# Kernel optimization log

Measured on AMD Instinct MI355X. Metric: run time of the kernel, lower is better.

Reference implementation:

```python
import jax, jax.numpy as jnp
import numpy as np
from jax import lax

V, E, H, K, T, B = 32000, 512, 512, 32, 256, 64
PAD_W = 0          # word_dict['PAD']
START, END, PAD_L = 30, 31, 0   # label_dict
NEG = -100000.0


def setup_inputs() -> dict:
    key = jax.random.key(0)
    ks = jax.random.split(key, 12)
    s = 1.0 / np.sqrt(H)
    tokens = jax.random.randint(ks[0], (T, B), 1, V, dtype=jnp.int32)   # >PAD_W -> mask all ones
    tags = jax.random.randint(ks[1], (T, B), 1, K - 2, dtype=jnp.int32)
    lengths = jnp.full((B,), T, dtype=jnp.int32)
    embed = jax.random.normal(ks[2], (V, E), jnp.float32) * 0.1
    wih0 = jax.random.uniform(ks[3], (2, 4 * H, E), jnp.float32, -s, s)
    whh0 = jax.random.uniform(ks[4], (2, 4 * H, H), jnp.float32, -s, s)
    b0 = jax.random.uniform(ks[5], (2, 4 * H), jnp.float32, -s, s)
    wih1 = jax.random.uniform(ks[6], (2, 4 * H, 2 * H), jnp.float32, -s, s)
    whh1 = jax.random.uniform(ks[7], (2, 4 * H, H), jnp.float32, -s, s)
    b1 = jax.random.uniform(ks[8], (2, 4 * H), jnp.float32, -s, s)
    lin_w = jax.random.uniform(ks[9], (K, 2 * H), jnp.float32, -s, s)
    lin_b = jax.random.uniform(ks[10], (K,), jnp.float32, -s, s)
    trans = jax.random.normal(ks[11], (K, K), jnp.float32)
    # replicate the torch transition init (same order of assignments)
    trans = trans.at[START, :].set(NEG)
    trans = trans.at[:, END].set(NEG)
    trans = trans.at[:, PAD_L].set(NEG)
    trans = trans.at[PAD_L, :].set(NEG)
    trans = trans.at[PAD_L, END].set(0.0)
    trans = trans.at[PAD_L, PAD_L].set(0.0)
    return dict(tokens=tokens, tags=tags, lengths=lengths, embed=embed,
                wih0=wih0, whh0=whh0, b0=b0, wih1=wih1, whh1=whh1, b1=b1,
                lin_w=lin_w, lin_b=lin_b, trans=trans)


def _lstm_dir(x, w_ih, w_hh, b, reverse):
    # x: [T,B,in] -> hs: [T,B,H]; gates precomputed as one big GEMM
    xp = jnp.einsum('tbi,gi->tbg', x, w_ih) + b  # [T,B,4H]
    h0 = jnp.zeros((x.shape[1], H), x.dtype)

    def step(carry, g_in):
        h, c = carry
        g = g_in + h @ w_hh.T
        i, f, gg, o = jnp.split(g, 4, axis=-1)  # torch gate order i,f,g,o
        c = jax.nn.sigmoid(f) * c + jax.nn.sigmoid(i) * jnp.tanh(gg)
        h = jax.nn.sigmoid(o) * jnp.tanh(c)
        return (h, c), h

    _, hs = lax.scan(step, (h0, h0), xp, reverse=reverse)
    return hs


def _bilstm_layer(x, wih, whh, b):
    return jnp.concatenate([_lstm_dir(x, wih[0], whh[0], b[0], False),
                            _lstm_dir(x, wih[1], whh[1], b[1], True)], axis=-1)


def reference(tokens, tags, lengths, embed, wih0, whh0, b0, wih1, whh1, b1,
              lin_w, lin_b, trans):
    mask = (tokens > PAD_W).astype(jnp.float32)  # [T,B]
    x = embed[tokens]                            # [T,B,E]
    x = _bilstm_layer(x, wih0, whh0, b0)
    x = _bilstm_layer(x, wih1, whh1, b1)
    feats = x @ lin_w.T + lin_b                  # [T,B,K]

    nB = tokens.shape[1]
    # ---- CRF forward algorithm: log Z(x) ----
    init = jnp.full((nB, K), NEG, feats.dtype).at[:, START].set(0.0)

    def step(score, inp):
        emit, m = inp  # [B,K], [B]
        # new[b,k] = logsumexp_j(score[b,j] + trans[k,j]) + emit[b,k]
        new = jax.nn.logsumexp(score[:, None, :] + trans[None, :, :], axis=2) + emit
        return jnp.where(m[:, None] > 0, new, score), None

    z, _ = lax.scan(step, init, (feats, mask))
    log_z = jax.nn.logsumexp(z + trans[END][None, :], axis=1)  # [B]

    # ---- gold path score (vectorized, masked deltas sum) ----
    start_row = jnp.full((1, nB), START, dtype=tags.dtype)
    te = jnp.concatenate([start_row, tags], axis=0)            # [T+1,B]
    trans_s = trans[te[1:], te[:-1]]                           # [T,B]
    emit_s = jnp.take_along_axis(feats, te[1:][..., None].astype(jnp.int32), axis=2)[..., 0]
    gold = jnp.sum(mask * (trans_s + emit_s), axis=0) + trans[END, te[-1]]

    return jnp.sum((log_z - gold) / lengths.astype(jnp.float32))
```

## Files before the change

kernel.cpp:

```cpp
#include <hip/hip_runtime.h>
#include <math.h>

#define T_STEPS 256
#define BATCH   64
#define HID     512
#define KTAGS   32
#define NEGV    -100000.0f
#define START_TAG 30
#define END_TAG   31

#define NBLK      256
#define SPIN_LIM  (1 << 26)
#define LAYER_DONE  300u
#define POISON_DONE 301u
#define POISON    0xFFFFFFFFFFFFFFFFULL

typedef __attribute__((ext_vector_type(8))) short short8;
typedef __attribute__((ext_vector_type(4))) float f32x4;

union V16 { uint4 u; short8 s; };
union HQ  { unsigned long long q[2]; short8 s; };

static __device__ __forceinline__ unsigned short f2b(float f) {
    unsigned u = __float_as_uint(f);
    return (unsigned short)((u + 0x7fffu + ((u >> 16) & 1u)) >> 16);
}
static __device__ __forceinline__ float b2f(unsigned short us) {
    return __uint_as_float(((unsigned)us) << 16);
}

__global__ __launch_bounds__(256) void init_zero(unsigned int* __restrict__ flags,
                                                 unsigned long long* __restrict__ hbuf,
                                                 float* __restrict__ out)
{
    int i = blockIdx.x * 256 + threadIdx.x;
    if (i < 131072)
        __hip_atomic_store(hbuf + i, POISON, __ATOMIC_RELAXED, __HIP_MEMORY_SCOPE_AGENT);
    if (i < 16384)
        __hip_atomic_store(flags + i, 0u, __ATOMIC_RELAXED, __HIP_MEMORY_SCOPE_AGENT);
    if (i == 0)
        __hip_atomic_store(out, 0.0f, __ATOMIC_RELAXED, __HIP_MEMORY_SCOPE_AGENT);
}

__global__ __launch_bounds__(256) void convert_embed(const float* __restrict__ src,
                                                     unsigned short* __restrict__ dst)
{
    long long i = ((long long)blockIdx.x * 256 + threadIdx.x) * 4;
    if (i >= (long long)32000 * 512) return;
    float4 v = *(const float4*)(src + i);
    ushort4 o;
    o.x = f2b(v.x); o.y = f2b(v.y); o.z = f2b(v.z); o.w = f2b(v.w);
    *(ushort4*)(dst + i) = o;
}

__global__ __launch_bounds__(256) void pack_w(const float* __restrict__ wih,
                                              const float* __restrict__ whh,
                                              int xK,
                                              unsigned short* __restrict__ wpack)
{
    const int xKt = xK >> 5, KT = xKt + 16;
    long long t = (long long)blockIdx.x * 256 + threadIdx.x;
    if (t >= (long long)2 * 64 * KT * 2 * 64) return;
    int lane = (int)(t & 63);
    long long rest = t >> 6;
    int nf = (int)(rest & 1); rest >>= 1;
    int kt = (int)(rest % KT); rest /= KT;
    int nt = (int)(rest % 64);
    int d  = (int)(rest / 64);
    int c = lane & 15, q = lane >> 4;
    int bc = nf * 16 + c;
    int r = (bc >> 3) * 512 + nt * 8 + (bc & 7);
    const float* src;
    if (kt < xKt) src = wih + ((long long)d * 2048 * xK + (long long)r * xK + kt * 32 + q * 8);
    else          src = whh + ((long long)d * 2048 * 512 + (long long)r * 512 + (kt - xKt) * 32 + q * 8);
    float4 v0 = *(const float4*)src;
    float4 v1 = *(const float4*)(src + 4);
    unsigned short o[8] = { f2b(v0.x), f2b(v0.y), f2b(v0.z), f2b(v0.w),
                            f2b(v1.x), f2b(v1.y), f2b(v1.z), f2b(v1.w) };
    *(uint4*)(wpack + t * 8) = *(const uint4*)o;
}

__global__ __launch_bounds__(256) void lstm_mfma(
    const int* __restrict__ tokens,
    const unsigned short* __restrict__ embB,
    const unsigned short* __restrict__ wp0,
    const unsigned short* __restrict__ wp1,
    const float* __restrict__ bb0, const float* __restrict__ bb1,
    unsigned short* __restrict__ hs0,
    unsigned short* __restrict__ hs1,
    unsigned long long* __restrict__ hbuf64,
    unsigned int* __restrict__ flags)
{
    __shared__ uint4 wldsH[2048];
    __shared__ float Gred[4][32][33];
    __shared__ float hsh[32][9];
    __shared__ int   tok_s[32];

    const int bid = blockIdx.x;
    const int d   = bid >> 7;
    const int bg  = (bid >> 6) & 1;
    const int nt  = bid & 63;
    const int tid = threadIdx.x;
    const int w    = tid >> 6;
    const int lane = tid & 63;
    const int lm = lane & 15, q = lane >> 4;
    const int brow = tid >> 3, hc = tid & 7;

    float creg = 0.0f;

    for (int l = 0; l < 2; ++l) {
        const int xK  = l ? 1024 : 512;
        const int xKt = xK >> 5;
        const int KT  = xKt + 16;
        const int nX  = xKt >> 2;
        const unsigned short* wp = (l ? wp1 : wp0) + (long long)(d * 64 + nt) * KT * 1024;
        const float* bia = (l ? bb1 : bb0) + (long long)d * 2048;
        unsigned short* hso = l ? hs1 : hs0;

        const uint4* wp4 = (const uint4*)wp;
        for (int j = tid; j < 2048; j += 256)
            wldsH[j] = wp4[xKt * 128 + j];

        float breg[4];
        #pragma unroll
        for (int g = 0; g < 4; ++g) breg[g] = bia[g * 512 + nt * 8 + hc];
        creg = 0.0f;
        __syncthreads();

        for (int s = 0; s < T_STEPS; ++s) {
            const int tt = d ? (T_STEPS - 1 - s) : s;

            if (l == 0 && tid < 32) tok_s[tid] = tokens[tt * BATCH + bg * 32 + tid];
            __syncthreads();

            HQ hq[4][2];
            const unsigned long long* hbq =
                hbuf64 + (long long)(((((s - 1) & 7) * 2 + d) * 2 + bg)) * 4096;
            if (s > 0) {
                #pragma unroll
                for (int i = 0; i < 4; ++i) {
                    const int kth = w * 4 + i;
                    #pragma unroll
                    for (int mt = 0; mt < 2; ++mt) {
                        const int base = (kth * 4 + q) * 64 + (mt * 16 + lm) * 2;
                        hq[i][mt].q[0] = __hip_atomic_load(hbq + base,     __ATOMIC_RELAXED, __HIP_MEMORY_SCOPE_AGENT);
                        hq[i][mt].q[1] = __hip_atomic_load(hbq + base + 1, __ATOMIC_RELAXED, __HIP_MEMORY_SCOPE_AGENT);
                    }
                }
            }

            f32x4 acc[2][2];
            #pragma unroll
            for (int mt = 0; mt < 2; ++mt)
                #pragma unroll
                for (int nf = 0; nf < 2; ++nf) acc[mt][nf] = (f32x4)0.0f;

            const unsigned short* xr[2];
            #pragma unroll
            for (int mt = 0; mt < 2; ++mt) {
                int m = mt * 16 + lm;
                if (l == 0) xr[mt] = embB + (long long)tok_s[m] * 512;
                else        xr[mt] = hs0 + ((long long)tt * 64 + bg * 32 + m) * 1024;
            }

            for (int i = 0; i < nX; ++i) {
                const int kt = w * nX + i;
                V16 av[2], bv[2];
                #pragma unroll
                for (int mt = 0; mt < 2; ++mt)
                    av[mt].u = *(const uint4*)(xr[mt] + kt * 32 + q * 8);
                #pragma unroll
                for (int nf = 0; nf < 2; ++nf)
                    bv[nf].u = *(const uint4*)(wp + ((long long)kt * 128 + nf * 64 + lane) * 8);
                #pragma unroll
                for (int mt = 0; mt < 2; ++mt)
                    #pragma unroll
                    for (int nf = 0; nf < 2; ++nf)
                        acc[mt][nf] = __builtin_amdgcn_mfma_f32_16x16x32_bf16(av[mt].s, bv[nf].s, acc[mt][nf], 0, 0, 0);
            }

            if (s > 0) {
                int n = 0;
                for (;;) {
                    int bad = 0;
                    #pragma unroll
                    for (int i = 0; i < 4; ++i) {
                        const int kth = w * 4 + i;
                        #pragma unroll
                        for (int mt = 0; mt < 2; ++mt) {
                            const int base = (kth * 4 + q) * 64 + (mt * 16 + lm) * 2;
                            if (hq[i][mt].q[0] == POISON) {
                                hq[i][mt].q[0] = __hip_atomic_load(hbq + base,     __ATOMIC_RELAXED, __HIP_MEMORY_SCOPE_AGENT);
                                bad = 1;
                            }
                            if (hq[i][mt].q[1] == POISON) {
                                hq[i][mt].q[1] = __hip_atomic_load(hbq + base + 1, __ATOMIC_RELAXED, __HIP_MEMORY_SCOPE_AGENT);
                                bad = 1;
                            }
                        }
                    }
                    if (!bad) break;
                    __builtin_amdgcn_s_sleep(1);
                    if (++n > SPIN_LIM) break;
                }

                #pragma unroll
                for (int i = 0; i < 4; ++i) {
                    const int kth = w * 4 + i;
                    V16 bv[2];
                    #pragma unroll
                    for (int nf = 0; nf < 2; ++nf)
                        bv[nf].u = wldsH[(kth * 2 + nf) * 64 + lane];
                    #pragma unroll
                    for (int mt = 0; mt < 2; ++mt)
                        #pragma unroll
                        for (int nf = 0; nf < 2; ++nf)
                            acc[mt][nf] = __builtin_amdgcn_mfma_f32_16x16x32_bf16(hq[i][mt].s, bv[nf].s, acc[mt][nf], 0, 0, 0);
                }
            }

            #pragma unroll
            for (int mt = 0; mt < 2; ++mt)
                #pragma unroll
                for (int nf = 0; nf < 2; ++nf)
                    #pragma unroll
                    for (int r = 0; r < 4; ++r)
                        Gred[w][nf * 16 + lm][mt * 16 + q * 4 + r] = acc[mt][nf][r];
            __syncthreads();

            float vg[4];
            #pragma unroll
            for (int g = 0; g < 4; ++g) {
                float v = breg[g];
                #pragma unroll
                for (int ww = 0; ww < 4; ++ww) v += Gred[ww][g * 8 + hc][brow];
                vg[g] = v;
            }
            const float si = 1.0f / (1.0f + __expf(-vg[0]));
            const float sf = 1.0f / (1.0f + __expf(-vg[1]));
            const float so = 1.0f / (1.0f + __expf(-vg[3]));
            const float cn = sf * creg + si * tanhf(vg[2]);
            const float hn = so * tanhf(cn);
            creg = cn;
            hsh[brow][hc] = hn;
            __syncthreads();

            if (tid < 64) {
                const int row = tid >> 1, cq = tid & 1;
                unsigned long long hv =
                      (unsigned long long)f2b(hsh[row][cq * 4 + 0])
                    | ((unsigned long long)f2b(hsh[row][cq * 4 + 1]) << 16)
                    | ((unsigned long long)f2b(hsh[row][cq * 4 + 2]) << 32)
                    | ((unsigned long long)f2b(hsh[row][cq * 4 + 3]) << 48);
                unsigned long long* dst =
                    hbuf64 + ((long long)((((s & 7) * 2 + d) * 2 + bg) * 64 + nt)) * 64 + tid;
                __hip_atomic_store(dst, hv, __ATOMIC_RELAXED, __HIP_MEMORY_SCOPE_AGENT);
                *(unsigned long long*)(hso + ((long long)tt * 64 + bg * 32 + row) * 1024
                                           + d * 512 + nt * 8 + cq * 4) = hv;
                unsigned long long* pdst =
                    hbuf64 + ((long long)(((((s + 2) & 7) * 2 + d) * 2 + bg) * 64 + nt)) * 64 + tid;
                __hip_atomic_store(pdst, POISON, __ATOMIC_RELAXED, __HIP_MEMORY_SCOPE_AGENT);
            }
        }

        if (l == 0) {
            __threadfence();
            __syncthreads();
            if (tid == 0)
                __hip_atomic_store(flags + bid * 32, LAYER_DONE,
                                   __ATOMIC_RELAXED, __HIP_MEMORY_SCOPE_AGENT);
            if (tid < 64) {
                int n = 0;
                for (;;) {
                    unsigned a = __hip_atomic_load(flags + tid * 32,         __ATOMIC_RELAXED, __HIP_MEMORY_SCOPE_AGENT);
                    unsigned b = __hip_atomic_load(flags + (tid + 64) * 32,  __ATOMIC_RELAXED, __HIP_MEMORY_SCOPE_AGENT);
                    unsigned c = __hip_atomic_load(flags + (tid + 128) * 32, __ATOMIC_RELAXED, __HIP_MEMORY_SCOPE_AGENT);
                    unsigned e = __hip_atomic_load(flags + (tid + 192) * 32, __ATOMIC_RELAXED, __HIP_MEMORY_SCOPE_AGENT);
                    if (__all(a >= LAYER_DONE && b >= LAYER_DONE &&
                              c >= LAYER_DONE && e >= LAYER_DONE)) break;
                    __builtin_amdgcn_s_sleep(1);
                    if (++n > SPIN_LIM) break;
                }
            }
            __syncthreads();
            if (tid < 64) {
                #pragma unroll
                for (int p = 0; p < 8; ++p) {
                    unsigned long long* pd =
                        hbuf64 + ((long long)(((p * 2 + d) * 2 + bg) * 64 + nt)) * 64 + tid;
                    __hip_atomic_store(pd, POISON, __ATOMIC_RELAXED, __HIP_MEMORY_SCOPE_AGENT);
                }
            }
            asm volatile("s_waitcnt vmcnt(0)" ::: "memory");
            __syncthreads();
            if (tid == 0)
                __hip_atomic_store(flags + bid * 32, POISON_DONE,
                                   __ATOMIC_RELAXED, __HIP_MEMORY_SCOPE_AGENT);
            if (tid < 64) {
                int n = 0;
                for (;;) {
                    unsigned a = __hip_atomic_load(flags + tid * 32,         __ATOMIC_RELAXED, __HIP_MEMORY_SCOPE_AGENT);
                    unsigned b = __hip_atomic_load(flags + (tid + 64) * 32,  __ATOMIC_RELAXED, __HIP_MEMORY_SCOPE_AGENT);
                    unsigned c = __hip_atomic_load(flags + (tid + 128) * 32, __ATOMIC_RELAXED, __HIP_MEMORY_SCOPE_AGENT);
                    unsigned e = __hip_atomic_load(flags + (tid + 192) * 32, __ATOMIC_RELAXED, __HIP_MEMORY_SCOPE_AGENT);
                    if (__all(a >= POISON_DONE && b >= POISON_DONE &&
                              c >= POISON_DONE && e >= POISON_DONE)) break;
                    __builtin_amdgcn_s_sleep(1);
                    if (++n > SPIN_LIM) break;
                }
            }
            __syncthreads();
            __threadfence();
        }
    }
}

__global__ __launch_bounds__(256) void gemm_feats(
    const unsigned short* __restrict__ A,
    const float* __restrict__ W,
    const float* __restrict__ bias,
    float* __restrict__ C,
    int M, int N, int K)
{
    __shared__ __align__(16) float As[64][34];
    __shared__ __align__(16) float Ws[32][68];

    const int m0 = blockIdx.y * 64;
    const int tid = threadIdx.x;
    const int tr = tid >> 4;
    const int tc = tid & 15;

    float acc[4][4];
    #pragma unroll
    for (int i = 0; i < 4; ++i)
        #pragma unroll
        for (int j = 0; j < 4; ++j) acc[i][j] = 0.0f;

    for (int k0 = 0; k0 < K; k0 += 32) {
        {
            int row = tid >> 2, g8 = tid & 3;
            uint4 v = *(const uint4*)(A + ((long long)(m0 + row)) * 1024 + k0 + g8 * 8);
            const unsigned short* pv = (const unsigned short*)&v;
            #pragma unroll
            for (int e = 0; e < 8; ++e) As[row][g8 * 8 + e] = b2f(pv[e]);
        }
        {
            int row = tid >> 3, q2 = tid & 7;
            float4 v = *(const float4*)(W + (long long)row * K + k0 + 4 * q2);
            Ws[4*q2+0][row] = v.x; Ws[4*q2+1][row] = v.y;
            Ws[4*q2+2][row] = v.z; Ws[4*q2+3][row] = v.w;
        }
        __syncthreads();
        #pragma unroll 8
        for (int kk = 0; kk < 32; ++kk) {
            float a0 = As[4*tr+0][kk], a1 = As[4*tr+1][kk];
            float a2 = As[4*tr+2][kk], a3 = As[4*tr+3][kk];
            float4 wv = *(const float4*)&Ws[kk][4*tc];
            acc[0][0] += a0*wv.x; acc[0][1] += a0*wv.y; acc[0][2] += a0*wv.z; acc[0][3] += a0*wv.w;
            acc[1][0] += a1*wv.x; acc[1][1] += a1*wv.y; acc[1][2] += a1*wv.z; acc[1][3] += a1*wv.w;
            acc[2][0] += a2*wv.x; acc[2][1] += a2*wv.y; acc[2][2] += a2*wv.z; acc[2][3] += a2*wv.w;
            acc[3][0] += a3*wv.x; acc[3][1] += a3*wv.y; acc[3][2] += a3*wv.z; acc[3][3] += a3*wv.w;
        }
        __syncthreads();
    }
    #pragma unroll
    for (int i = 0; i < 4; ++i) {
        int m = m0 + 4*tr + i;
        #pragma unroll
        for (int j = 0; j < 4; ++j) {
            int n = 4*tc + j;
            if (n < N) C[(long long)m * N + n] = acc[i][j] + bias[n];
        }
    }
}

__global__ __launch_bounds__(1024) void crf_kernel(
    const float* __restrict__ feats,
    const float* __restrict__ trans,
    const int*   __restrict__ tokens,
    const int*   __restrict__ tags,
    const int*   __restrict__ lengths,
    float* __restrict__ out)
{
    const int b = blockIdx.x;
    const int tid = threadIdx.x;
    __shared__ float tr_s[KTAGS*KTAGS];
    __shared__ float score_s[KTAGS];
    __shared__ float emit_s[KTAGS];
    __shared__ float red_s[16];
    __shared__ float logz_s;

    tr_s[tid] = trans[tid];
    if (tid < KTAGS) score_s[tid] = (tid == START_TAG) ? 0.0f : NEGV;
    __syncthreads();

    const int i = tid >> 5, j = tid & 31;
    for (int t = 0; t < T_STEPS; ++t) {
        if (tid < KTAGS) emit_s[tid] = feats[((long long)t*BATCH + b)*KTAGS + tid];
        __syncthreads();
        float e = score_s[j] + tr_s[i*KTAGS + j];
        float m = e;
        m = fmaxf(m, __shfl_xor(m, 1));  m = fmaxf(m, __shfl_xor(m, 2));
        m = fmaxf(m, __shfl_xor(m, 4));  m = fmaxf(m, __shfl_xor(m, 8));
        m = fmaxf(m, __shfl_xor(m, 16));
        float p = __expf(e - m);
        p += __shfl_xor(p, 1); p += __shfl_xor(p, 2); p += __shfl_xor(p, 4);
        p += __shfl_xor(p, 8); p += __shfl_xor(p, 16);
        float nv = m + __logf(p) + emit_s[i];
        int msk = tokens[(long long)t*BATCH + b] > 0;
        __syncthreads();
        if (j == 0) score_s[i] = msk ? nv : score_s[i];
        __syncthreads();
    }

    if (tid < KTAGS) {
        float v = score_s[tid] + tr_s[END_TAG*KTAGS + tid];
        float m = v;
        m = fmaxf(m, __shfl_xor(m, 1));  m = fmaxf(m, __shfl_xor(m, 2));
        m = fmaxf(m, __shfl_xor(m, 4));  m = fmaxf(m, __shfl_xor(m, 8));
        m = fmaxf(m, __shfl_xor(m, 16));
        float p = __expf(v - m);
        p += __shfl_xor(p, 1); p += __shfl_xor(p, 2); p += __shfl_xor(p, 4);
        p += __shfl_xor(p, 8); p += __shfl_xor(p, 16);
        if (tid == 0) logz_s = m + __logf(p);
    }
    __syncthreads();

    float val = 0.0f;
    if (tid < T_STEPS) {
        int t = tid;
        int cur  = tags[(long long)t*BATCH + b];
        int prev = (t == 0) ? START_TAG : tags[(long long)(t-1)*BATCH + b];
        int msk  = tokens[(long long)t*BATCH + b] > 0;
        if (msk) val = tr_s[cur*KTAGS + prev]
                     + feats[((long long)t*BATCH + b)*KTAGS + cur];
    }
    val += __shfl_xor(val, 1);  val += __shfl_xor(val, 2);
    val += __shfl_xor(val, 4);  val += __shfl_xor(val, 8);
    val += __shfl_xor(val, 16); val += __shfl_xor(val, 32);
    int wave = tid >> 6, lane = tid & 63;
    if (lane == 0) red_s[wave] = val;
    __syncthreads();
    if (tid == 0) {
        float g = 0.0f;
        #pragma unroll
        for (int w = 0; w < 16; ++w) g += red_s[w];
        g += tr_s[END_TAG*KTAGS + tags[(long long)(T_STEPS-1)*BATCH + b]];
        atomicAdd(out, (logz_s - g) / (float)lengths[b]);
    }
}

extern "C" void kernel_launch(void* const* d_in, const int* in_sizes, int n_in,
                              void* d_out, int out_size, void* d_ws, size_t ws_size,
                              hipStream_t stream) {
    const int*   tokens  = (const int*)  d_in[0];
    const int*   tags    = (const int*)  d_in[1];
    const int*   lengths = (const int*)  d_in[2];
    const float* embed   = (const float*)d_in[3];
    const float* wih0    = (const float*)d_in[4];
    const float* whh0    = (const float*)d_in[5];
    const float* b0      = (const float*)d_in[6];
    const float* wih1    = (const float*)d_in[7];
    const float* whh1    = (const float*)d_in[8];
    const float* b1      = (const float*)d_in[9];
    const float* lin_w   = (const float*)d_in[10];
    const float* lin_b   = (const float*)d_in[11];
    const float* trans   = (const float*)d_in[12];

    char* ws = (char*)d_ws;
    unsigned short* hs0   = (unsigned short*)(ws);
    unsigned short* hs1   = (unsigned short*)(ws +  33554432ULL);
    unsigned short* embB  = (unsigned short*)(ws +  67108864ULL);
    unsigned short* wp0   = (unsigned short*)(ws +  99876864ULL);
    unsigned short* wp1   = (unsigned short*)(ws + 108265472ULL);
    float*          feats = (float*)        (ws + 120848384ULL);
    unsigned int*   flagsP = (unsigned int*)feats;
    unsigned long long* hbufP = (unsigned long long*)((char*)feats + 65536);

    float* out = (float*)d_out;

    init_zero<<<dim3(512), 256, 0, stream>>>(flagsP, hbufP, out);
    convert_embed<<<dim3(16000), 256, 0, stream>>>(embed, embB);
    pack_w<<<dim3(2048), 256, 0, stream>>>(wih0, whh0, 512,  wp0);
    pack_w<<<dim3(3072), 256, 0, stream>>>(wih1, whh1, 1024, wp1);

    lstm_mfma<<<dim3(NBLK), 256, 0, stream>>>(
        tokens, embB, wp0, wp1, b0, b1, hs0, hs1, hbufP, flagsP);

    gemm_feats<<<dim3(1, 256, 1), 256, 0, stream>>>(
        hs1, lin_w, lin_b, feats, T_STEPS*BATCH, KTAGS, 2*HID);

    crf_kernel<<<dim3(BATCH), 1024, 0, stream>>>(feats, trans, tokens, tags,
                                                 lengths, out);
}
```

Measured before the change: 2.859 ms.

## Template LSTM layer steps, prefetch input operands, and pack h via shuffles

Splits the per-layer recurrence into a template specialized on input width, so the x-projection loop is fully unrolled. All input and weight fragments are issued as loads before the h-buffer loads and MFMAs. The hidden-state packing now uses warp shuffles instead of a shared-memory stage plus an extra __syncthreads per step. The goal is to shorten the serial critical path of each timestep, at the cost of higher register pressure from holding all prefetched operands (launch_bounds now asks for one block per CU).

```diff
diff --git a/kernel.cpp b/kernel.cpp
--- a/kernel.cpp
+++ b/kernel.cpp
@@ -80,7 +80,179 @@
     *(uint4*)(wpack + t * 8) = *(const uint4*)o;
 }
 
-__global__ __launch_bounds__(256) void lstm_mfma(
+template<int XK>
+static __device__ __forceinline__ void layer_steps(
+    const int d, const int bg, const int nt, const int tid,
+    const int* __restrict__ tokens,
+    const unsigned short* __restrict__ embB,
+    const unsigned short* __restrict__ hs_in,
+    const unsigned short* __restrict__ wp,
+    const float* __restrict__ bia,
+    unsigned short* __restrict__ hso,
+    unsigned long long* __restrict__ hbuf64,
+    uint4* __restrict__ wldsH,
+    float (&Gred)[4][32][33],
+    int* __restrict__ tok_s)
+{
+    constexpr bool L0  = (XK == 512);
+    constexpr int  xKt = XK >> 5;
+    constexpr int  nX  = xKt >> 2;
+
+    const int w = tid >> 6, lane = tid & 63;
+    const int lm = lane & 15, q = lane >> 4;
+    const int brow = tid >> 3, hc = tid & 7;
+
+    const uint4* wp4 = (const uint4*)wp;
+    for (int j = tid; j < 2048; j += 256)
+        wldsH[j] = wp4[xKt * 128 + j];
+
+    float breg[4];
+    #pragma unroll
+    for (int g = 0; g < 4; ++g) breg[g] = bia[g * 512 + nt * 8 + hc];
+    float creg = 0.0f;
+
+    __syncthreads();
+
+    for (int s = 0; s < T_STEPS; ++s) {
+        const int tt = d ? (T_STEPS - 1 - s) : s;
+
+        if (L0 && tid < 32) tok_s[tid] = tokens[tt * BATCH + bg * 32 + tid];
+        __syncthreads();
+
+        const unsigned short* xr[2];
+        #pragma unroll
+        for (int mt = 0; mt < 2; ++mt) {
+            int m = mt * 16 + lm;
+            if (L0) xr[mt] = embB + (long long)tok_s[m] * 512;
+            else    xr[mt] = hs_in + ((long long)tt * 64 + bg * 32 + m) * 1024;
+        }
+
+        uint4 av[nX][2], bv[nX][2];
+        #pragma unroll
+        for (int i = 0; i < nX; ++i) {
+            const int kt = w * nX + i;
+            #pragma unroll
+            for (int mt = 0; mt < 2; ++mt)
+                av[i][mt] = *(const uint4*)(xr[mt] + kt * 32 + q * 8);
+            #pragma unroll
+            for (int nf = 0; nf < 2; ++nf)
+                bv[i][nf] = *(const uint4*)(wp + ((long long)kt * 128 + nf * 64 + lane) * 8);
+        }
+
+        HQ hq[4][2];
+        const unsigned long long* hbq =
+            hbuf64 + (long long)(((((s - 1) & 7) * 2 + d) * 2 + bg)) * 4096;
+        if (s > 0) {
+            #pragma unroll
+            for (int i = 0; i < 4; ++i) {
+                const int kth = w * 4 + i;
+                #pragma unroll
+                for (int mt = 0; mt < 2; ++mt) {
+                    const int base = (kth * 4 + q) * 64 + (mt * 16 + lm) * 2;
+                    hq[i][mt].q[0] = __hip_atomic_load(hbq + base,     __ATOMIC_RELAXED, __HIP_MEMORY_SCOPE_AGENT);
+                    hq[i][mt].q[1] = __hip_atomic_load(hbq + base + 1, __ATOMIC_RELAXED, __HIP_MEMORY_SCOPE_AGENT);
+                }
+            }
+        }
+
+        f32x4 acc[2][2];
+        #pragma unroll
+        for (int mt = 0; mt < 2; ++mt)
+            #pragma unroll
+            for (int nf = 0; nf < 2; ++nf) acc[mt][nf] = (f32x4)0.0f;
+
+        #pragma unroll
+        for (int i = 0; i < nX; ++i) {
+            V16 a0, a1, b0, b1;
+            a0.u = av[i][0]; a1.u = av[i][1];
+            b0.u = bv[i][0]; b1.u = bv[i][1];
+            acc[0][0] = __builtin_amdgcn_mfma_f32_16x16x32_bf16(a0.s, b0.s, acc[0][0], 0, 0, 0);
+            acc[0][1] = __builtin_amdgcn_mfma_f32_16x16x32_bf16(a0.s, b1.s, acc[0][1], 0, 0, 0);
+            acc[1][0] = __builtin_amdgcn_mfma_f32_16x16x32_bf16(a1.s, b0.s, acc[1][0], 0, 0, 0);
+            acc[1][1] = __builtin_amdgcn_mfma_f32_16x16x32_bf16(a1.s, b1.s, acc[1][1], 0, 0, 0);
+        }
+
+        if (s > 0) {
+            int n = 0;
+            for (;;) {
+                int bad = 0;
+                #pragma unroll
+                for (int i = 0; i < 4; ++i) {
+                    const int kth = w * 4 + i;
+                    #pragma unroll
+                    for (int mt = 0; mt < 2; ++mt) {
+                        const int base = (kth * 4 + q) * 64 + (mt * 16 + lm) * 2;
+                        if (hq[i][mt].q[0] == POISON) {
+                            hq[i][mt].q[0] = __hip_atomic_load(hbq + base,     __ATOMIC_RELAXED, __HIP_MEMORY_SCOPE_AGENT);
+                            bad = 1;
+                        }
+                        if (hq[i][mt].q[1] == POISON) {
+                            hq[i][mt].q[1] = __hip_atomic_load(hbq + base + 1, __ATOMIC_RELAXED, __HIP_MEMORY_SCOPE_AGENT);
+                            bad = 1;
+                        }
+                    }
+                }
+                if (!bad) break;
+                __builtin_amdgcn_s_sleep(1);
+                if (++n > SPIN_LIM) break;
+            }
+
+            #pragma unroll
+            for (int i = 0; i < 4; ++i) {
+                const int kth = w * 4 + i;
+                V16 b0, b1;
+                b0.u = wldsH[(kth * 2 + 0) * 64 + lane];
+                b1.u = wldsH[(kth * 2 + 1) * 64 + lane];
+                acc[0][0] = __builtin_amdgcn_mfma_f32_16x16x32_bf16(hq[i][0].s, b0.s, acc[0][0], 0, 0, 0);
+                acc[0][1] = __builtin_amdgcn_mfma_f32_16x16x32_bf16(hq[i][0].s, b1.s, acc[0][1], 0, 0, 0);
+                acc[1][0] = __builtin_amdgcn_mfma_f32_16x16x32_bf16(hq[i][1].s, b0.s, acc[1][0], 0, 0, 0);
+                acc[1][1] = __builtin_amdgcn_mfma_f32_16x16x32_bf16(hq[i][1].s, b1.s, acc[1][1], 0, 0, 0);
+            }
+        }
+
+        #pragma unroll
+        for (int mt = 0; mt < 2; ++mt)
+            #pragma unroll
+            for (int nf = 0; nf < 2; ++nf)
+                #pragma unroll
+                for (int r = 0; r < 4; ++r)
+                    Gred[w][nf * 16 + lm][mt * 16 + q * 4 + r] = acc[mt][nf][r];
+        __syncthreads();
+
+        float vg[4];
+        #pragma unroll
+        for (int g = 0; g < 4; ++g) {
+            float v = breg[g];
+            #pragma unroll
+            for (int ww = 0; ww < 4; ++ww) v += Gred[ww][g * 8 + hc][brow];
+            vg[g] = v;
+        }
+        const float si = 1.0f / (1.0f + __expf(-vg[0]));
+        const float sf = 1.0f / (1.0f + __expf(-vg[1]));
+        const float so = 1.0f / (1.0f + __expf(-vg[3]));
+        const float cn = sf * creg + si * tanhf(vg[2]);
+        const float hn = so * tanhf(cn);
+        creg = cn;
+
+        unsigned pv = (unsigned)f2b(hn);
+        unsigned p2 = pv | (__shfl_xor(pv, 1) << 16);
+        unsigned long long hv = (unsigned long long)p2
+                              | ((unsigned long long)__shfl_xor(p2, 2) << 32);
+        if ((tid & 3) == 0) {
+            const int row = brow, cq = hc >> 2;
+            unsigned long long* dst =
+                hbuf64 + ((long long)((((s & 7) * 2 + d) * 2 + bg) * 64 + nt)) * 64 + row * 2 + cq;
+            __hip_atomic_store(dst, hv, __ATOMIC_RELAXED, __HIP_MEMORY_SCOPE_AGENT);
+            *(unsigned long long*)(hso + ((long long)tt * 64 + bg * 32 + row) * 1024
+                                       + d * 512 + nt * 8 + cq * 4) = hv;
+            unsigned long long* pdst =
+                hbuf64 + ((long long)(((((s + 2) & 7) * 2 + d) * 2 + bg) * 64 + nt)) * 64 + row * 2 + cq;
+            __hip_atomic_store(pdst, POISON, __ATOMIC_RELAXED, __HIP_MEMORY_SCOPE_AGENT);
+        }
+    }
+}
+
+__global__ __launch_bounds__(256, 1) void lstm_mfma(
     const int* __restrict__ tokens,
     const unsigned short* __restrict__ embB,
     const unsigned short* __restrict__ wp0,
@@ -93,7 +265,6 @@
 {
     __shared__ uint4 wldsH[2048];
     __shared__ float Gred[4][32][33];
-    __shared__ float hsh[32][9];
     __shared__ int   tok_s[32];
 
     const int bid = blockIdx.x;
@@ -101,218 +272,66 @@
     const int bg  = (bid >> 6) & 1;
     const int nt  = bid & 63;
     const int tid = threadIdx.x;
-    const int w    = tid >> 6;
-    const int lane = tid & 63;
-    const int lm = lane & 15, q = lane >> 4;
-    const int brow = tid >> 3, hc = tid & 7;
-
-    float creg = 0.0f;
-
-    for (int l = 0; l < 2; ++l) {
-        const int xK  = l ? 1024 : 512;
-        const int xKt = xK >> 5;
-        const int KT  = xKt + 16;
-        const int nX  = xKt >> 2;
-        const unsigned short* wp = (l ? wp1 : wp0) + (long long)(d * 64 + nt) * KT * 1024;
-        const float* bia = (l ? bb1 : bb0) + (long long)d * 2048;
-        unsigned short* hso = l ? hs1 : hs0;
-
-        const uint4* wp4 = (const uint4*)wp;
-        for (int j = tid; j < 2048; j += 256)
-            wldsH[j] = wp4[xKt * 128 + j];
-
-        float breg[4];
-        #pragma unroll
-        for (int g = 0; g < 4; ++g) breg[g] = bia[g * 512 + nt * 8 + hc];
-        creg = 0.0f;
-        __syncthreads();
-
-        for (int s = 0; s < T_STEPS; ++s) {
-            const int tt = d ? (T_STEPS - 1 - s) : s;
-
-            if (l == 0 && tid < 32) tok_s[tid] = tokens[tt * BATCH + bg * 32 + tid];
-            __syncthreads();
-
-            HQ hq[4][2];
-            const unsigned long long* hbq =
-                hbuf64 + (long long)(((((s - 1) & 7) * 2 + d) * 2 + bg)) * 4096;
-            if (s > 0) {
-                #pragma unroll
-                for (int i = 0; i < 4; ++i) {
-                    const int kth = w * 4 + i;
-                    #pragma unroll
-                    for (int mt = 0; mt < 2; ++mt) {
-                        const int base = (kth * 4 + q) * 64 + (mt * 16 + lm) * 2;
-                        hq[i][mt].q[0] = __hip_atomic_load(hbq + base,     __ATOMIC_RELAXED, __HIP_MEMORY_SCOPE_AGENT);
-                        hq[i][mt].q[1] = __hip_atomic_load(hbq + base + 1, __ATOMIC_RELAXED, __HIP_MEMORY_SCOPE_AGENT);
-                    }
-                }
+
+    layer_steps<512>(d, bg, nt, tid, tokens, embB, (const unsigned short*)nullptr,
+                     wp0 + (long long)(d * 64 + nt) * 32 * 1024,
+                     bb0 + (long long)d * 2048,
+                     hs0, hbuf64, wldsH, Gred, tok_s);
+
+    {
+        __threadfence();
+        __syncthreads();
+        if (tid == 0)
+            __hip_atomic_store(flags + bid * 32, LAYER_DONE,
+                               __ATOMIC_RELAXED, __HIP_MEMORY_SCOPE_AGENT);
+        if (tid < 64) {
+            int n = 0;
+            for (;;) {
+                unsigned a = __hip_atomic_load(flags + tid * 32,         __ATOMIC_RELAXED, __HIP_MEMORY_SCOPE_AGENT);
+                unsigned b = __hip_atomic_load(flags + (tid + 64) * 32,  __ATOMIC_RELAXED, __HIP_MEMORY_SCOPE_AGENT);
+                unsigned c = __hip_atomic_load(flags + (tid + 128) * 32, __ATOMIC_RELAXED, __HIP_MEMORY_SCOPE_AGENT);
+                unsigned e = __hip_atomic_load(flags + (tid + 192) * 32, __ATOMIC_RELAXED, __HIP_MEMORY_SCOPE_AGENT);
+                if (__all(a >= LAYER_DONE && b >= LAYER_DONE &&
+                          c >= LAYER_DONE && e >= LAYER_DONE)) break;
+                __builtin_amdgcn_s_sleep(1);
+                if (++n > SPIN_LIM) break;
             }
-
-            f32x4 acc[2][2];
-            #pragma unroll
-            for (int mt = 0; mt < 2; ++mt)
-                #pragma unroll
-                for (int nf = 0; nf < 2; ++nf) acc[mt][nf] = (f32x4)0.0f;
-
-            const unsigned short* xr[2];
-            #pragma unroll
-            for (int mt = 0; mt < 2; ++mt) {
-                int m = mt * 16 + lm;
-                if (l == 0) xr[mt] = embB + (long long)tok_s[m] * 512;
-                else        xr[mt] = hs0 + ((long long)tt * 64 + bg * 32 + m) * 1024;
+        }
+        __syncthreads();
+        if (tid < 64) {
+            #pragma unroll
+            for (int p = 0; p < 8; ++p) {
+                unsigned long long* pd =
+                    hbuf64 + ((long long)(((p * 2 + d) * 2 + bg) * 64 + nt)) * 64 + tid;
+                __hip_atomic_store(pd, POISON, __ATOMIC_RELAXED, __HIP_MEMORY_SCOPE_AGENT);
             }
-
-            for (int i = 0; i < nX; ++i) {
-                const int kt = w * nX + i;
-                V16 av[2], bv[2];
-                #pragma unroll
-                for (int mt = 0; mt < 2; ++mt)
-                    av[mt].u = *(const uint4*)(xr[mt] + kt * 32 + q * 8);
-                #pragma unroll
-                for (int nf = 0; nf < 2; ++nf)
-                    bv[nf].u = *(const uint4*)(wp + ((long long)kt * 128 + nf * 64 + lane) * 8);
-                #pragma unroll
-                for (int mt = 0; mt < 2; ++mt)
-                    #pragma unroll
-                    for (int nf = 0; nf < 2; ++nf)
-                        acc[mt][nf] = __builtin_amdgcn_mfma_f32_16x16x32_bf16(av[mt].s, bv[nf].s, acc[mt][nf], 0, 0, 0);
+        }
+        asm volatile("s_waitcnt vmcnt(0)" ::: "memory");
+        __syncthreads();
+        if (tid == 0)
+            __hip_atomic_store(flags + bid * 32, POISON_DONE,
+                               __ATOMIC_RELAXED, __HIP_MEMORY_SCOPE_AGENT);
+        if (tid < 64) {
+            int n = 0;
+            for (;;) {
+                unsigned a = __hip_atomic_load(flags + tid * 32,         __ATOMIC_RELAXED, __HIP_MEMORY_SCOPE_AGENT);
+                unsigned b = __hip_atomic_load(flags + (tid + 64) * 32,  __ATOMIC_RELAXED, __HIP_MEMORY_SCOPE_AGENT);
+                unsigned c = __hip_atomic_load(flags + (tid + 128) * 32, __ATOMIC_RELAXED, __HIP_MEMORY_SCOPE_AGENT);
+                unsigned e = __hip_atomic_load(flags + (tid + 192) * 32, __ATOMIC_RELAXED, __HIP_MEMORY_SCOPE_AGENT);
+                if (__all(a >= POISON_DONE && b >= POISON_DONE &&
+                          c >= POISON_DONE && e >= POISON_DONE)) break;
+                __builtin_amdgcn_s_sleep(1);
+                if (++n > SPIN_LIM) break;
             }
-
-            if (s > 0) {
-                int n = 0;
-                for (;;) {
-                    int bad = 0;
-                    #pragma unroll
-                    for (int i = 0; i < 4; ++i) {
-                        const int kth = w * 4 + i;
-                        #pragma unroll
-                        for (int mt = 0; mt < 2; ++mt) {
-                            const int base = (kth * 4 + q) * 64 + (mt * 16 + lm) * 2;
-                            if (hq[i][mt].q[0] == POISON) {
-                                hq[i][mt].q[0] = __hip_atomic_load(hbq + base,     __ATOMIC_RELAXED, __HIP_MEMORY_SCOPE_AGENT);
-                                bad = 1;
-                            }
-                            if (hq[i][mt].q[1] == POISON) {
-                                hq[i][mt].q[1] = __hip_atomic_load(hbq + base + 1, __ATOMIC_RELAXED, __HIP_MEMORY_SCOPE_AGENT);
-                                bad = 1;
-                            }
-                        }
-                    }
-                    if (!bad) break;
-                    __builtin_amdgcn_s_sleep(1);
-                    if (++n > SPIN_LIM) break;
-                }
-
-                #pragma unroll
-                for (int i = 0; i < 4; ++i) {
-                    const int kth = w * 4 + i;
-                    V16 bv[2];
-                    #pragma unroll
-                    for (int nf = 0; nf < 2; ++nf)
-                        bv[nf].u = wldsH[(kth * 2 + nf) * 64 + lane];
-                    #pragma unroll
-                    for (int mt = 0; mt < 2; ++mt)
-                        #pragma unroll
-                        for (int nf = 0; nf < 2; ++nf)
-                            acc[mt][nf] = __builtin_amdgcn_mfma_f32_16x16x32_bf16(hq[i][mt].s, bv[nf].s, acc[mt][nf], 0, 0, 0);
-                }
-            }
-
-            #pragma unroll
-            for (int mt = 0; mt < 2; ++mt)
-                #pragma unroll
-                for (int nf = 0; nf < 2; ++nf)
-                    #pragma unroll
-                    for (int r = 0; r < 4; ++r)
-                        Gred[w][nf * 16 + lm][mt * 16 + q * 4 + r] = acc[mt][nf][r];
-            __syncthreads();
-
-            float vg[4];
-            #pragma unroll
-            for (int g = 0; g < 4; ++g) {
-                float v = breg[g];
-                #pragma unroll
-                for (int ww = 0; ww < 4; ++ww) v += Gred[ww][g * 8 + hc][brow];
-                vg[g] = v;
-            }
-            const float si = 1.0f / (1.0f + __expf(-vg[0]));
-            const float sf = 1.0f / (1.0f + __expf(-vg[1]));
-            const float so = 1.0f / (1.0f + __expf(-vg[3]));
-            const float cn = sf * creg + si * tanhf(vg[2]);
-            const float hn = so * tanhf(cn);
-            creg = cn;
-            hsh[brow][hc] = hn;
-            __syncthreads();
-
-            if (tid < 64) {
-                const int row = tid >> 1, cq = tid & 1;
-                unsigned long long hv =
-                      (unsigned long long)f2b(hsh[row][cq * 4 + 0])
-                    | ((unsigned long long)f2b(hsh[row][cq * 4 + 1]) << 16)
-                    | ((unsigned long long)f2b(hsh[row][cq * 4 + 2]) << 32)
-                    | ((unsigned long long)f2b(hsh[row][cq * 4 + 3]) << 48);
-                unsigned long long* dst =
-                    hbuf64 + ((long long)((((s & 7) * 2 + d) * 2 + bg) * 64 + nt)) * 64 + tid;
-                __hip_atomic_store(dst, hv, __ATOMIC_RELAXED, __HIP_MEMORY_SCOPE_AGENT);
-                *(unsigned long long*)(hso + ((long long)tt * 64 + bg * 32 + row) * 1024
-                                           + d * 512 + nt * 8 + cq * 4) = hv;
-                unsigned long long* pdst =
-                    hbuf64 + ((long long)(((((s + 2) & 7) * 2 + d) * 2 + bg) * 64 + nt)) * 64 + tid;
-                __hip_atomic_store(pdst, POISON, __ATOMIC_RELAXED, __HIP_MEMORY_SCOPE_AGENT);
-            }
-        }
-
-        if (l == 0) {
-            __threadfence();
-            __syncthreads();
-            if (tid == 0)
-                __hip_atomic_store(flags + bid * 32, LAYER_DONE,
-                                   __ATOMIC_RELAXED, __HIP_MEMORY_SCOPE_AGENT);
-            if (tid < 64) {
-                int n = 0;
-                for (;;) {
-                    unsigned a = __hip_atomic_load(flags + tid * 32,         __ATOMIC_RELAXED, __HIP_MEMORY_SCOPE_AGENT);
-                    unsigned b = __hip_atomic_load(flags + (tid + 64) * 32,  __ATOMIC_RELAXED, __HIP_MEMORY_SCOPE_AGENT);
-                    unsigned c = __hip_atomic_load(flags + (tid + 128) * 32, __ATOMIC_RELAXED, __HIP_MEMORY_SCOPE_AGENT);
-                    unsigned e = __hip_atomic_load(flags + (tid + 192) * 32, __ATOMIC_RELAXED, __HIP_MEMORY_SCOPE_AGENT);
-                    if (__all(a >= LAYER_DONE && b >= LAYER_DONE &&
-                              c >= LAYER_DONE && e >= LAYER_DONE)) break;
-                    __builtin_amdgcn_s_sleep(1);
-                    if (++n > SPIN_LIM) break;
-                }
-            }
-            __syncthreads();
-            if (tid < 64) {
-                #pragma unroll
-                for (int p = 0; p < 8; ++p) {
-                    unsigned long long* pd =
-                        hbuf64 + ((long long)(((p * 2 + d) * 2 + bg) * 64 + nt)) * 64 + tid;
-                    __hip_atomic_store(pd, POISON, __ATOMIC_RELAXED, __HIP_MEMORY_SCOPE_AGENT);
-                }
-            }
-            asm volatile("s_waitcnt vmcnt(0)" ::: "memory");
-            __syncthreads();
-            if (tid == 0)
-                __hip_atomic_store(flags + bid * 32, POISON_DONE,
-                                   __ATOMIC_RELAXED, __HIP_MEMORY_SCOPE_AGENT);
-            if (tid < 64) {
-                int n = 0;
-                for (;;) {
-                    unsigned a = __hip_atomic_load(flags + tid * 32,         __ATOMIC_RELAXED, __HIP_MEMORY_SCOPE_AGENT);
-                    unsigned b = __hip_atomic_load(flags + (tid + 64) * 32,  __ATOMIC_RELAXED, __HIP_MEMORY_SCOPE_AGENT);
-                    unsigned c = __hip_atomic_load(flags + (tid + 128) * 32, __ATOMIC_RELAXED, __HIP_MEMORY_SCOPE_AGENT);
-                    unsigned e = __hip_atomic_load(flags + (tid + 192) * 32, __ATOMIC_RELAXED, __HIP_MEMORY_SCOPE_AGENT);
-                    if (__all(a >= POISON_DONE && b >= POISON_DONE &&
-                              c >= POISON_DONE && e >= POISON_DONE)) break;
-                    __builtin_amdgcn_s_sleep(1);
-                    if (++n > SPIN_LIM) break;
-                }
-            }
-            __syncthreads();
-            __threadfence();
-        }
-    }
+        }
+        __syncthreads();
+        __threadfence();
+    }
+
+    layer_steps<1024>(d, bg, nt, tid, tokens, embB, hs0,
+                      wp1 + (long long)(d * 64 + nt) * 48 * 1024,
+                      bb1 + (long long)d * 2048,
+                      hs1, hbuf64, wldsH, Gred, tok_s);
 }
 
 __global__ __launch_bounds__(256) void gemm_feats(
```

Measured after the change: 2.424 ms. -15.2%, faster.
